# Kernel optimization log

Hardware: AMD Instinct MI355X
Metric: run time of the kernel (lower is better)

Reference implementation:

```python
import jax, jax.numpy as jnp
import numpy as np

EPS = 1e-5
FT_DEPTH = 5
FT_SMOOTH = 1e-5


def _conv(x, w):
    # x: [B,H,W,Cin], w: [kh,kw,Cin,Cout], SAME padding, stride 1
    return jax.lax.conv_general_dilated(x, w, (1, 1), 'SAME',
                                         dimension_numbers=('NHWC', 'HWIO', 'NHWC'))


def _bn(x, g, b, m, v):
    # inference-mode batch norm over last axis
    return (x - m) * jax.lax.rsqrt(v + EPS) * g + b


def _ftanimoto(p, l, axis):
    # Fractal Tanimoto similarity with keepdims, averaged over FT_DEPTH scales.
    tpl = jnp.sum(p * l, axis=axis, keepdims=True)
    tpp = jnp.sum(p * p, axis=axis, keepdims=True)
    tll = jnp.sum(l * l, axis=axis, keepdims=True)
    num = tpl + FT_SMOOTH
    denum = jnp.zeros_like(tpl)
    for d in range(FT_DEPTH):
        a = 2.0 ** d
        b = -(2.0 * a - 1.0)
        denum = denum + 1.0 / (a * (tpp + tll) + b * tpl + FT_SMOOTH)
    return num * denum * (1.0 / FT_DEPTH)


def setup_inputs() -> dict:
    key = jax.random.key(0)
    ks = jax.random.split(key, 24)
    B, H, W, C = 8, 128, 128, 96
    d = {}
    d['x1'] = jax.random.normal(ks[0], (B, H, W, C), jnp.float32)
    d['x2'] = jax.random.normal(ks[1], (B, H, W, C), jnp.float32)
    d['x3'] = jax.random.normal(ks[2], (B, H, W, C), jnp.float32)
    d['wq'] = jax.random.normal(ks[3], (3, 3, C, C), jnp.float32) * 0.05
    d['gq'] = jax.random.uniform(ks[4], (C,), jnp.float32)
    d['bq'] = jax.random.normal(ks[5], (C,), jnp.float32) * 0.1
    d['mq'] = jax.random.normal(ks[6], (C,), jnp.float32) * 0.1
    d['vq'] = jax.random.uniform(ks[7], (C,), jnp.float32) + 0.5
    d['wk'] = jax.random.normal(ks[8], (3, 3, C, C), jnp.float32) * 0.05
    d['gk'] = jax.random.uniform(ks[9], (C,), jnp.float32)
    d['bk'] = jax.random.normal(ks[10], (C,), jnp.float32) * 0.1
    d['mk'] = jax.random.normal(ks[11], (C,), jnp.float32) * 0.1
    d['vk'] = jax.random.uniform(ks[12], (C,), jnp.float32) + 0.5
    d['wv'] = jax.random.normal(ks[13], (3, 3, C, C), jnp.float32) * 0.05
    d['gv'] = jax.random.uniform(ks[14], (C,), jnp.float32)
    d['bv'] = jax.random.normal(ks[15], (C,), jnp.float32) * 0.1
    d['mv'] = jax.random.normal(ks[16], (C,), jnp.float32) * 0.1
    d['vv'] = jax.random.uniform(ks[17], (C,), jnp.float32) + 0.5
    d['gn'] = jax.random.uniform(ks[18], (C,), jnp.float32)
    d['bnb'] = jax.random.normal(ks[19], (C,), jnp.float32) * 0.1
    d['mn'] = jax.random.normal(ks[20], (C,), jnp.float32) * 0.1
    d['vn'] = jax.random.uniform(ks[21], (C,), jnp.float32) + 0.5
    return d


def reference(x1, x2, x3, wq, gq, bq, mq, vq, wk, gk, bk, mk, vk,
              wv, gv, bv, mv, vv, gn, bnb, mn, vn):
    q = jax.nn.sigmoid(_bn(_conv(x1, wq), gq, bq, mq, vq))   # [B,H,W,C]
    k = jax.nn.sigmoid(_bn(_conv(x2, wk), gk, bk, mk, vk))
    v = jax.nn.sigmoid(_bn(_conv(x3, wv), gv, bv, mv, vv))
    att_spat = _ftanimoto(q, k, axis=-1)        # [B,H,W,1] spatial attention
    att_chan = _ftanimoto(q, k, axis=(1, 2))    # [B,1,1,C] channel attention
    v_cspat = 0.5 * (att_chan * v + att_spat * v)
    return _bn(v_cspat, gn, bnb, mn, vn)
```

## Files before the change

kernel.cpp:

```cpp
#include <hip/hip_runtime.h>
#include <hip/hip_bf16.h>
#include <math.h>

#define BB 8
#define HH 128
#define WW 128
#define CC 96
#define NPIX (BB*HH*WW)
#define EPSF 1e-5f
#define FT_SMOOTH_F 1e-5f
#define ROWB 8320
#define WELEM 82944

typedef short short8 __attribute__((ext_vector_type(8)));
typedef float f32x4 __attribute__((ext_vector_type(4)));

__device__ __forceinline__ float ftanimoto(float tpl, float tpp, float tll) {
    float num = tpl + FT_SMOOTH_F;
    float denum = 0.0f;
    float a = 1.0f;
#pragma unroll
    for (int d = 0; d < 5; ++d) {
        float bco = -(2.0f * a - 1.0f);
        denum += 1.0f / (a * (tpp + tll) + bco * tpl + FT_SMOOTH_F);
        a *= 2.0f;
    }
    return num * denum * 0.2f;
}

__device__ __forceinline__ unsigned short f2bf(float f) {
    __hip_bfloat16 h = __float2bfloat16(f);
    return *(unsigned short*)&h;
}

__device__ __forceinline__ float bf2f(unsigned short u) {
    return __uint_as_float((unsigned int)u << 16);
}

__global__ __launch_bounds__(256) void cast_wT2(
    const float* __restrict__ wq, const float* __restrict__ wk,
    const float* __restrict__ wv, unsigned short* __restrict__ wT2)
{
    const int tid = blockIdx.x * 256 + threadIdx.x;
    if (tid >= 3 * WELEM) return;
    const int cid = tid / WELEM;
    const int o = tid - cid * WELEM;
    const int j = o & 7;
    const int rest = o >> 3;
    const int lq = rest & 63;
    const int lrow = lq >> 2, qq = lq & 3;
    const int tile = rest >> 6;
    const int nt = tile % 6;
    const int tcc = tile / 6;
    const int cc = tcc % 3, tap = tcc / 3;
    const int ci = cc * 32 + qq * 8 + j;
    const int co = nt * 16 + lrow;
    const float* w = (cid == 0) ? wq : (cid == 1) ? wk : wv;
    wT2[tid] = f2bf(w[(size_t)(tap * CC + ci) * CC + co]);
}

__global__ __launch_bounds__(256, 3) void conv_all(
    const float* __restrict__ x1, const float* __restrict__ x2,
    const float* __restrict__ x3, const unsigned short* __restrict__ wT2,
    const float* __restrict__ gq, const float* __restrict__ bq,
    const float* __restrict__ mq, const float* __restrict__ vq,
    const float* __restrict__ gk, const float* __restrict__ bk,
    const float* __restrict__ mk, const float* __restrict__ vk,
    const float* __restrict__ gv, const float* __restrict__ bv,
    const float* __restrict__ mv, const float* __restrict__ vv,
    unsigned short* __restrict__ qb, unsigned short* __restrict__ kb,
    unsigned short* __restrict__ vb)
{
    __shared__ __align__(16) char smem[4 * ROWB];
    const int tid = threadIdx.x;
    const int wv = tid >> 6;
    const int L  = tid & 63;
    const int cid = blockIdx.x >> 9;
    const int blk = blockIdx.x & 511;
    const int b  = blk >> 6;
    const int h0 = (blk & 63) << 1;
    const int hrow = h0 + (wv >> 1);
    const int wwbase = (wv & 1) << 6;
    const int lrow = L & 15;
    const int qq = L >> 4;

    const float* xsrc = (cid == 0) ? x1 : (cid == 1) ? x2 : x3;
    const unsigned short* wT2p = wT2 + (size_t)cid * WELEM;

    const int hst = h0 - 1 + wv;
    const bool stv = (hst >= 0) && (hst < HH);
    const float* xrow = xsrc + (size_t)(b * HH + (stv ? hst : 0)) * WW * CC;
    char* myrow = smem + wv * ROWB;

    f32x4 acc[4][6];
#pragma unroll
    for (int mt = 0; mt < 4; ++mt)
#pragma unroll
        for (int nt = 0; nt < 6; ++nt) acc[mt][nt] = (f32x4){0.f, 0.f, 0.f, 0.f};

    for (int cc = 0; cc < 3; ++cc) {
        __syncthreads();
        if (stv) {
#pragma unroll
            for (int it = 0; it < 9; ++it) {
                const int idx = it * 64 + L;
                if (idx < 520) {
                    const int p = idx >> 2;
                    const int c = idx & 3;
                    const int w = p - 1;
                    short8 o = (short8){0,0,0,0,0,0,0,0};
                    if (w >= 0 && w < WW) {
                        const float* src = xrow + (size_t)w * CC + cc * 32 + c * 8;
                        const float4 a0 = *(const float4*)src;
                        const float4 a1 = *(const float4*)(src + 4);
                        o[0] = (short)f2bf(a0.x); o[1] = (short)f2bf(a0.y);
                        o[2] = (short)f2bf(a0.z); o[3] = (short)f2bf(a0.w);
                        o[4] = (short)f2bf(a1.x); o[5] = (short)f2bf(a1.y);
                        o[6] = (short)f2bf(a1.z); o[7] = (short)f2bf(a1.w);
                    }
                    const int slot = c ^ ((p ^ (p >> 2)) & 3);
                    *(short8*)(myrow + p * 64 + slot * 16) = o;
                }
            }
        }
        __syncthreads();
#pragma unroll
        for (int dy = -1; dy <= 1; ++dy) {
            const int hh = hrow + dy;
            if (hh < 0 || hh >= HH) continue;
            const char* ldsrow = smem + (dy + 1 + (wv >> 1)) * ROWB;
#pragma unroll
            for (int dx = -1; dx <= 1; ++dx) {
                const int tap = (dy + 1) * 3 + (dx + 1);
                const unsigned short* bsrc = wT2p + (size_t)(tap * 3 + cc) * 6 * 512;
                short8 bf[6];
#pragma unroll
                for (int nt = 0; nt < 6; ++nt)
                    bf[nt] = *(const short8*)(bsrc + nt * 512 + (lrow * 4 + qq) * 8);
                short8 af[4];
#pragma unroll
                for (int mt = 0; mt < 4; ++mt) {
                    const int p = wwbase + mt * 16 + lrow + dx + 1;
                    const int slot = qq ^ ((p ^ (p >> 2)) & 3);
                    af[mt] = *(const short8*)(ldsrow + p * 64 + slot * 16);
                }
#pragma unroll
                for (int nt = 0; nt < 6; ++nt)
#pragma unroll
                    for (int mt = 0; mt < 4; ++mt)
                        acc[mt][nt] = __builtin_amdgcn_mfma_f32_16x16x32_bf16(
                            af[mt], bf[nt], acc[mt][nt], 0, 0, 0);
            }
        }
    }

    const float* g  = (cid == 0) ? gq : (cid == 1) ? gk : gv;
    const float* bt = (cid == 0) ? bq : (cid == 1) ? bk : bv;
    const float* mu = (cid == 0) ? mq : (cid == 1) ? mk : mv;
    const float* var = (cid == 0) ? vq : (cid == 1) ? vk : vv;
    unsigned short* outp = (cid == 0) ? qb : (cid == 1) ? kb : vb;

#pragma unroll
    for (int nt = 0; nt < 6; ++nt) {
        const int co = nt * 16 + lrow;
        const float scl = g[co] * rsqrtf(var[co] + EPSF);
        const float sft = bt[co] - mu[co] * scl;
#pragma unroll
        for (int mt = 0; mt < 4; ++mt) {
#pragma unroll
            for (int r = 0; r < 4; ++r) {
                const int row = (wv << 6) + (mt << 4) + (qq << 2) + r;
                const int h = h0 + (row >> 7);
                const int w = row & 127;
                const size_t pix = (size_t)(b * HH + h) * WW + w;
                const float t = acc[mt][nt][r] * scl + sft;
                const float e = __builtin_amdgcn_exp2f(t * -1.442695041f);
                outp[pix * CC + co] = f2bf(__builtin_amdgcn_rcpf(1.0f + e));
            }
        }
    }
}

__global__ __launch_bounds__(192) void qk_att(
    const unsigned short* __restrict__ qb, const unsigned short* __restrict__ kb,
    float* __restrict__ atts, float* __restrict__ part)
{
    __shared__ float pxr[128][37];
    __shared__ float red[16][12][24];
    const int t = threadIdx.x;
    const int g = t / 12;
    const int c8 = t - g * 12;
    const size_t p0 = (size_t)blockIdx.x * 128;

    float s_tpl[8], s_tpp[8], s_tll[8];
#pragma unroll
    for (int j = 0; j < 8; ++j) { s_tpl[j] = 0.f; s_tpp[j] = 0.f; s_tll[j] = 0.f; }

#pragma unroll
    for (int i = 0; i < 8; ++i) {
        const int px = g + i * 16;
        const size_t pe = (p0 + px) * CC + c8 * 8;
        const short8 qv = *(const short8*)(qb + pe);
        const short8 kv = *(const short8*)(kb + pe);
        float ptpl = 0.f, ptpp = 0.f, ptll = 0.f;
#pragma unroll
        for (int j = 0; j < 8; ++j) {
            const float qf = bf2f((unsigned short)qv[j]);
            const float kf = bf2f((unsigned short)kv[j]);
            s_tpl[j] = fmaf(qf, kf, s_tpl[j]);
            s_tpp[j] = fmaf(qf, qf, s_tpp[j]);
            s_tll[j] = fmaf(kf, kf, s_tll[j]);
            ptpl = fmaf(qf, kf, ptpl);
            ptpp = fmaf(qf, qf, ptpp);
            ptll = fmaf(kf, kf, ptll);
        }
        pxr[px][c8 * 3 + 0] = ptpl;
        pxr[px][c8 * 3 + 1] = ptpp;
        pxr[px][c8 * 3 + 2] = ptll;
    }
#pragma unroll
    for (int j = 0; j < 8; ++j) {
        red[g][c8][j]      = s_tpl[j];
        red[g][c8][8 + j]  = s_tpp[j];
        red[g][c8][16 + j] = s_tll[j];
    }
    __syncthreads();

    if (t < 128) {
        float tpl = 0.f, tpp = 0.f, tll = 0.f;
#pragma unroll
        for (int c = 0; c < 12; ++c) {
            tpl += pxr[t][c * 3 + 0];
            tpp += pxr[t][c * 3 + 1];
            tll += pxr[t][c * 3 + 2];
        }
        atts[p0 + t] = ftanimoto(tpl, tpp, tll);
    }

    if (t < CC) {
        const int cg = t >> 3, cj = t & 7;
        float tpl = 0.f, tpp = 0.f, tll = 0.f;
        for (int gg = 0; gg < 16; ++gg) {
            tpl += red[gg][cg][cj];
            tpp += red[gg][cg][8 + cj];
            tll += red[gg][cg][16 + cj];
        }
        const size_t idx = ((size_t)blockIdx.x * CC + t) * 3;
        part[idx + 0] = tpl;
        part[idx + 1] = tpp;
        part[idx + 2] = tll;
    }
}

__global__ __launch_bounds__(256) void chan_final2(
    const float* __restrict__ part, float* __restrict__ attc)
{
    const int wid = blockIdx.x * 4 + (threadIdx.x >> 6);
    const int lane = threadIdx.x & 63;
    const int b = wid / CC;
    const int c = wid - b * CC;
    const size_t base = (((size_t)b * 128 + lane) * CC + c) * 3;
    const size_t off = (size_t)64 * CC * 3;
    float tpl = part[base + 0] + part[base + off + 0];
    float tpp = part[base + 1] + part[base + off + 1];
    float tll = part[base + 2] + part[base + off + 2];
#pragma unroll
    for (int off2 = 32; off2 > 0; off2 >>= 1) {
        tpl += __shfl_xor(tpl, off2);
        tpp += __shfl_xor(tpp, off2);
        tll += __shfl_xor(tll, off2);
    }
    if (lane == 0) attc[b * CC + c] = ftanimoto(tpl, tpp, tll);
}

__global__ __launch_bounds__(256) void final_combine(
    const unsigned short* __restrict__ vb, const float* __restrict__ atts,
    const float* __restrict__ attc,
    const float* __restrict__ gn, const float* __restrict__ bnb,
    const float* __restrict__ mn, const float* __restrict__ vn,
    float* __restrict__ out)
{
    const int tid = blockIdx.x * 256 + threadIdx.x;
    const int c8 = tid % 12;
    const int pix = tid / 12;
    const int b = pix >> 14;
    const short8 v = *(const short8*)(vb + (size_t)pix * CC + c8 * 8);
    const float as = atts[pix];
    float r[8];
#pragma unroll
    for (int j = 0; j < 8; ++j) {
        const int co = c8 * 8 + j;
        const float nscl = gn[co] * rsqrtf(vn[co] + EPSF);
        const float nsft = bnb[co] - mn[co] * nscl;
        const float att = 0.5f * (attc[b * CC + co] + as);
        r[j] = att * bf2f((unsigned short)v[j]) * nscl + nsft;
    }
    float* dst = out + (size_t)pix * CC + c8 * 8;
    *(float4*)dst = make_float4(r[0], r[1], r[2], r[3]);
    *(float4*)(dst + 4) = make_float4(r[4], r[5], r[6], r[7]);
}

extern "C" void kernel_launch(void* const* d_in, const int* in_sizes, int n_in,
                              void* d_out, int out_size, void* d_ws, size_t ws_size,
                              hipStream_t stream)
{
    const float* x1 = (const float*)d_in[0];
    const float* x2 = (const float*)d_in[1];
    const float* x3 = (const float*)d_in[2];
    const float* wq = (const float*)d_in[3];
    const float* gq = (const float*)d_in[4];
    const float* bq = (const float*)d_in[5];
    const float* mq = (const float*)d_in[6];
    const float* vq = (const float*)d_in[7];
    const float* wk = (const float*)d_in[8];
    const float* gk = (const float*)d_in[9];
    const float* bk = (const float*)d_in[10];
    const float* mk = (const float*)d_in[11];
    const float* vk = (const float*)d_in[12];
    const float* wvw = (const float*)d_in[13];
    const float* gv = (const float*)d_in[14];
    const float* bv = (const float*)d_in[15];
    const float* mv = (const float*)d_in[16];
    const float* vv = (const float*)d_in[17];
    const float* gn = (const float*)d_in[18];
    const float* bnb = (const float*)d_in[19];
    const float* mn = (const float*)d_in[20];
    const float* vn = (const float*)d_in[21];

    unsigned short* wT2 = (unsigned short*)d_ws;
    unsigned short* vb = wT2 + (size_t)3 * WELEM;
    float* atts = (float*)(vb + (size_t)NPIX * CC);
    float* part = atts + NPIX;
    float* attc = part + (size_t)1024 * CC * 3;

    unsigned short* qb = (unsigned short*)d_out;
    unsigned short* kb = qb + (size_t)NPIX * CC;

    cast_wT2<<<(3 * WELEM + 255) / 256, 256, 0, stream>>>(wq, wk, wvw, wT2);
    conv_all<<<1536, 256, 0, stream>>>(x1, x2, x3, wT2,
                                       gq, bq, mq, vq, gk, bk, mk, vk,
                                       gv, bv, mv, vv, qb, kb, vb);
    qk_att<<<NPIX / 128, 192, 0, stream>>>(qb, kb, atts, part);
    chan_final2<<<192, 256, 0, stream>>>(part, attc);
    final_combine<<<NPIX * 12 / 256, 256, 0, stream>>>(vb, atts, attc,
                                                       gn, bnb, mn, vn,
                                                       (float*)d_out);
}
```

Before: 326.0 us.

## Pre-cast inputs to bf16 and run conv directly from global memory

Adds a precast pass that converts x1/x2/x3 to bf16 in the workspace alongside the weight transpose. A new conv_direct kernel then loads the MFMA A-fragments straight from the bf16 global buffer instead of staging rows through LDS. The aim is to halve the conv's input read traffic and drop the LDS staging and barriers. In exchange it adds an extra full pass over the inputs and more workspace, and it depends on L2 to serve the overlapping tap reads. The old LDS path stays as a fallback when the workspace is too small.

```diff
diff --git a/kernel.cpp b/kernel.cpp
--- a/kernel.cpp
+++ b/kernel.cpp
@@ -11,6 +11,8 @@
 #define FT_SMOOTH_F 1e-5f
 #define ROWB 8320
 #define WELEM 82944
+#define WBLK 972
+#define XJOBS (3*NPIX*12)
 
 typedef short short8 __attribute__((ext_vector_type(8)));
 typedef float f32x4 __attribute__((ext_vector_type(4)));
@@ -37,29 +39,137 @@
     return __uint_as_float((unsigned int)u << 16);
 }
 
-__global__ __launch_bounds__(256) void cast_wT2(
+__global__ __launch_bounds__(256) void precast(
     const float* __restrict__ wq, const float* __restrict__ wk,
-    const float* __restrict__ wv, unsigned short* __restrict__ wT2)
-{
-    const int tid = blockIdx.x * 256 + threadIdx.x;
-    if (tid >= 3 * WELEM) return;
-    const int cid = tid / WELEM;
-    const int o = tid - cid * WELEM;
-    const int j = o & 7;
-    const int rest = o >> 3;
-    const int lq = rest & 63;
-    const int lrow = lq >> 2, qq = lq & 3;
-    const int tile = rest >> 6;
-    const int nt = tile % 6;
-    const int tcc = tile / 6;
-    const int cc = tcc % 3, tap = tcc / 3;
-    const int ci = cc * 32 + qq * 8 + j;
-    const int co = nt * 16 + lrow;
-    const float* w = (cid == 0) ? wq : (cid == 1) ? wk : wv;
-    wT2[tid] = f2bf(w[(size_t)(tap * CC + ci) * CC + co]);
-}
-
-__global__ __launch_bounds__(256, 3) void conv_all(
+    const float* __restrict__ wv, unsigned short* __restrict__ wT2,
+    const float* __restrict__ x1, const float* __restrict__ x2,
+    const float* __restrict__ x3, unsigned short* __restrict__ xb)
+{
+    if (blockIdx.x < WBLK) {
+        const int tid = blockIdx.x * 256 + threadIdx.x;
+        const int cid = tid / WELEM;
+        const int o = tid - cid * WELEM;
+        const int j = o & 7;
+        const int rest = o >> 3;
+        const int lq = rest & 63;
+        const int lrow = lq >> 2, qq = lq & 3;
+        const int tile = rest >> 6;
+        const int nt = tile % 6;
+        const int tcc = tile / 6;
+        const int cc = tcc % 3, tap = tcc / 3;
+        const int ci = cc * 32 + qq * 8 + j;
+        const int co = nt * 16 + lrow;
+        const float* w = (cid == 0) ? wq : (cid == 1) ? wk : wv;
+        wT2[tid] = f2bf(w[(size_t)(tap * CC + ci) * CC + co]);
+        return;
+    }
+    const int tid2 = (blockIdx.x - WBLK) * 256 + threadIdx.x;
+    const int cid = tid2 / (NPIX * 12);
+    const int rem = tid2 - cid * (NPIX * 12);
+    const float* xs = (cid == 0) ? x1 : (cid == 1) ? x2 : x3;
+    const float4 a0 = *(const float4*)(xs + (size_t)rem * 8);
+    const float4 a1 = *(const float4*)(xs + (size_t)rem * 8 + 4);
+    short8 o;
+    o[0] = (short)f2bf(a0.x); o[1] = (short)f2bf(a0.y);
+    o[2] = (short)f2bf(a0.z); o[3] = (short)f2bf(a0.w);
+    o[4] = (short)f2bf(a1.x); o[5] = (short)f2bf(a1.y);
+    o[6] = (short)f2bf(a1.z); o[7] = (short)f2bf(a1.w);
+    *(short8*)(xb + (size_t)cid * NPIX * CC + (size_t)rem * 8) = o;
+}
+
+__global__ __launch_bounds__(256, 3) void conv_direct(
+    const unsigned short* __restrict__ xb, const unsigned short* __restrict__ wT2,
+    const float* __restrict__ gq, const float* __restrict__ bq,
+    const float* __restrict__ mq, const float* __restrict__ vq,
+    const float* __restrict__ gk, const float* __restrict__ bk,
+    const float* __restrict__ mk, const float* __restrict__ vk,
+    const float* __restrict__ gv, const float* __restrict__ bv,
+    const float* __restrict__ mv, const float* __restrict__ vv,
+    unsigned short* __restrict__ qb, unsigned short* __restrict__ kb,
+    unsigned short* __restrict__ vb)
+{
+    const int tid = threadIdx.x;
+    const int wv = tid >> 6;
+    const int L  = tid & 63;
+    const int cid = blockIdx.x >> 9;
+    const int blk = blockIdx.x & 511;
+    const int b  = blk >> 6;
+    const int h0 = (blk & 63) << 1;
+    const int hrow = h0 + (wv >> 1);
+    const int wwbase = (wv & 1) << 6;
+    const int lrow = L & 15;
+    const int qq = L >> 4;
+
+    const unsigned short* xbc = xb + (size_t)cid * NPIX * CC;
+    const unsigned short* wT2p = wT2 + (size_t)cid * WELEM;
+
+    f32x4 acc[4][6];
+#pragma unroll
+    for (int mt = 0; mt < 4; ++mt)
+#pragma unroll
+        for (int nt = 0; nt < 6; ++nt) acc[mt][nt] = (f32x4){0.f, 0.f, 0.f, 0.f};
+
+    for (int cc = 0; cc < 3; ++cc) {
+#pragma unroll
+        for (int dy = -1; dy <= 1; ++dy) {
+            const int hh = hrow + dy;
+            if (hh < 0 || hh >= HH) continue;
+            const unsigned short* xrow =
+                xbc + ((size_t)(b * HH + hh) * WW) * CC + cc * 32 + qq * 8;
+#pragma unroll
+            for (int dx = -1; dx <= 1; ++dx) {
+                const int tap = (dy + 1) * 3 + (dx + 1);
+                const unsigned short* bsrc = wT2p + (size_t)(tap * 3 + cc) * 6 * 512;
+                short8 bf[6];
+#pragma unroll
+                for (int nt = 0; nt < 6; ++nt)
+                    bf[nt] = *(const short8*)(bsrc + nt * 512 + (lrow * 4 + qq) * 8);
+                short8 af[4];
+#pragma unroll
+                for (int mt = 0; mt < 4; ++mt) {
+                    const int w = wwbase + mt * 16 + lrow + dx;
+                    af[mt] = (w >= 0 && w < WW)
+                                 ? *(const short8*)(xrow + (size_t)w * CC)
+                                 : (short8){0,0,0,0,0,0,0,0};
+                }
+#pragma unroll
+                for (int nt = 0; nt < 6; ++nt)
+#pragma unroll
+                    for (int mt = 0; mt < 4; ++mt)
+                        acc[mt][nt] = __builtin_amdgcn_mfma_f32_16x16x32_bf16(
+                            af[mt], bf[nt], acc[mt][nt], 0, 0, 0);
+            }
+        }
+    }
+
+    const float* g  = (cid == 0) ? gq : (cid == 1) ? gk : gv;
+    const float* bt = (cid == 0) ? bq : (cid == 1) ? bk : bv;
+    const float* mu = (cid == 0) ? mq : (cid == 1) ? mk : mv;
+    const float* var = (cid == 0) ? vq : (cid == 1) ? vk : vv;
+    unsigned short* outp = (cid == 0) ? qb : (cid == 1) ? kb : vb;
+
+#pragma unroll
+    for (int nt = 0; nt < 6; ++nt) {
+        const int co = nt * 16 + lrow;
+        const float scl = g[co] * rsqrtf(var[co] + EPSF);
+        const float sft = bt[co] - mu[co] * scl;
+#pragma unroll
+        for (int mt = 0; mt < 4; ++mt) {
+#pragma unroll
+            for (int r = 0; r < 4; ++r) {
+                const int row = (wv << 6) + (mt << 4) + (qq << 2) + r;
+                const int h = h0 + (row >> 7);
+                const int w = row & 127;
+                const size_t pix = (size_t)(b * HH + h) * WW + w;
+                const float t = acc[mt][nt][r] * scl + sft;
+                const float e = __builtin_amdgcn_exp2f(t * -1.442695041f);
+                outp[pix * CC + co] = f2bf(__builtin_amdgcn_rcpf(1.0f + e));
+            }
+        }
+    }
+}
+
+__global__ __launch_bounds__(256, 3) void conv_all_lds(
     const float* __restrict__ x1, const float* __restrict__ x2,
     const float* __restrict__ x3, const unsigned short* __restrict__ wT2,
     const float* __restrict__ gq, const float* __restrict__ bq,
@@ -328,18 +438,33 @@
     const float* vn = (const float*)d_in[21];
 
     unsigned short* wT2 = (unsigned short*)d_ws;
-    unsigned short* vb = wT2 + (size_t)3 * WELEM;
+    unsigned short* xb = wT2 + (size_t)3 * WELEM;
+    unsigned short* vb = xb + (size_t)3 * NPIX * CC;
     float* atts = (float*)(vb + (size_t)NPIX * CC);
     float* part = atts + NPIX;
     float* attc = part + (size_t)1024 * CC * 3;
 
+    const size_t need = (size_t)((char*)(attc + 768) - (char*)d_ws);
+
     unsigned short* qb = (unsigned short*)d_out;
     unsigned short* kb = qb + (size_t)NPIX * CC;
 
-    cast_wT2<<<(3 * WELEM + 255) / 256, 256, 0, stream>>>(wq, wk, wvw, wT2);
-    conv_all<<<1536, 256, 0, stream>>>(x1, x2, x3, wT2,
-                                       gq, bq, mq, vq, gk, bk, mk, vk,
-                                       gv, bv, mv, vv, qb, kb, vb);
+    if (ws_size >= need) {
+        precast<<<WBLK + XJOBS / 256, 256, 0, stream>>>(wq, wk, wvw, wT2,
+                                                        x1, x2, x3, xb);
+        conv_direct<<<1536, 256, 0, stream>>>(xb, wT2,
+                                              gq, bq, mq, vq, gk, bk, mk, vk,
+                                              gv, bv, mv, vv, qb, kb, vb);
+    } else {
+        vb = wT2 + (size_t)3 * WELEM;
+        atts = (float*)(vb + (size_t)NPIX * CC);
+        part = atts + NPIX;
+        attc = part + (size_t)1024 * CC * 3;
+        precast<<<WBLK, 256, 0, stream>>>(wq, wk, wvw, wT2, x1, x2, x3, xb);
+        conv_all_lds<<<1536, 256, 0, stream>>>(x1, x2, x3, wT2,
+                                               gq, bq, mq, vq, gk, bk, mk, vk,
+                                               gv, bv, mv, vv, qb, kb, vb);
+    }
     qk_att<<<NPIX / 128, 192, 0, stream>>>(qb, kb, atts, part);
     chan_final2<<<192, 256, 0, stream>>>(part, attc);
     final_combine<<<NPIX * 12 / 256, 256, 0, stream>>>(vb, atts, attc,
```

After: 418.5 us. 28.4% more time.
